# Kernel optimization log

Hardware: AMD Instinct MI355X
Metric: run time of the kernel (lower is better)

The kernel has to match this reference:

```python
import jax, jax.numpy as jnp
import numpy as np
from jax import lax

B, CIN, CH, HW, K = 256, 256, 256, 16, 3


def setup_inputs() -> dict:
    key = jax.random.key(0)
    ks = jax.random.split(key, 9)
    s = 0.05
    return {
        "x": jax.random.normal(ks[0], (B, CIN, HW, HW), dtype=jnp.float32),
        "h": jax.random.normal(ks[1], (B, CH, HW, HW), dtype=jnp.float32),
        "c": jax.random.normal(ks[2], (B, CH, HW, HW), dtype=jnp.float32),
        # stacked x-branch conv weights for gates [i, f, c, o]; no bias (matches torch code)
        "Wx": jax.random.normal(ks[3], (4 * CH, CIN, K, K), dtype=jnp.float32) * s,
        # stacked h-branch conv weights for gates [i, f, c, o]; with bias
        "Wh": jax.random.normal(ks[4], (4 * CH, CH, K, K), dtype=jnp.float32) * s,
        "bh": jax.random.normal(ks[5], (4 * CH,), dtype=jnp.float32) * s,
        # peephole params (torch inits them to zeros; use small randn to exercise the math)
        "Wci": jax.random.normal(ks[6], (1, CH, HW, HW), dtype=jnp.float32) * s,
        "Wcf": jax.random.normal(ks[7], (1, CH, HW, HW), dtype=jnp.float32) * s,
        "Wco": jax.random.normal(ks[8], (1, CH, HW, HW), dtype=jnp.float32) * s,
    }


def _conv(x, w):
    # same-padding 2D conv, NCHW/OIHW
    return lax.conv_general_dilated(
        x, w, window_strides=(1, 1), padding="SAME",
        dimension_numbers=("NCHW", "OIHW", "NCHW"))


def reference(x, h, c, Wx, Wh, bh, Wci, Wcf, Wco):
    gx = _conv(x, Wx)                                   # [B, 4*CH, H, W]
    gh = _conv(h, Wh) + bh[None, :, None, None]         # [B, 4*CH, H, W]
    xi, xf, xc, xo = jnp.split(gx, 4, axis=1)
    hi, hf, hc, ho = jnp.split(gh, 4, axis=1)
    i_t = jax.nn.sigmoid(xi + hi + Wci * c)
    f_t = jax.nn.sigmoid(xf + hf + Wcf * c)
    c_t = f_t * c + i_t * jnp.tanh(xc + hc)
    o_t = jax.nn.sigmoid(xo + ho + Wco * c_t)
    h_t = o_t * jnp.tanh(c_t)
    return (h_t, c_t)
```

## Files before the change

### kernel.cpp

```cpp
#include <hip/hip_runtime.h>


typedef __bf16 bf16x8 __attribute__((ext_vector_type(8)));
typedef float f32x16 __attribute__((ext_vector_type(16)));

#define PLANE_B  20736u
#define XH_BYTES (4096u * PLANE_B)
#define OUT_HALF 16777216u

__device__ inline void gload_lds16(const void* g, void* l) {
    __builtin_amdgcn_global_load_lds(
        (const __attribute__((address_space(1))) void*)g,
        (__attribute__((address_space(3))) void*)l, 16, 0, 0);
}

__global__ __launch_bounds__(256) void xh_transform(
    const float* __restrict__ x, const float* __restrict__ hh,
    unsigned char* __restrict__ xh)
{
    int blk = blockIdx.x;
    int b = blk >> 4, ibk = blk & 15;
    const float* src = (ibk < 8) ? (x  + ((size_t)(b*256 + ibk*32)) * 256)
                                 : (hh + ((size_t)(b*256 + (ibk-8)*32)) * 256);
    int t = threadIdx.x;
    uint32_t w[16];
#pragma unroll
    for (int i = 0; i < 16; ++i) {
        __bf16 lo = (__bf16)src[(size_t)(2*i  )*256 + t];
        __bf16 hi = (__bf16)src[(size_t)(2*i+1)*256 + t];
        w[i] = (uint32_t)__builtin_bit_cast(unsigned short, lo)
             | ((uint32_t)__builtin_bit_cast(unsigned short, hi) << 16);
    }
    unsigned char* plane = xh + (size_t)blk * PLANE_B;
    int p = ((t >> 4) + 1)*18 + (t & 15) + 1;
    uint32_t key  = (uint32_t)(p & 7) << 4;
    uint32_t base = (uint32_t)p * 64u;
#pragma unroll
    for (int k = 0; k < 4; ++k)
        *(uint4*)(plane + ((base + 16u*k) ^ key)) =
            uint4{w[4*k], w[4*k+1], w[4*k+2], w[4*k+3]};
    if (t < 68) {
        int pb;
        if      (t < 18) pb = t;
        else if (t < 36) pb = 17*18 + (t - 18);
        else if (t < 52) pb = (t - 35)*18;
        else             pb = (t - 51)*18 + 17;
        uint32_t kb = (uint32_t)(pb & 7) << 4;
        uint32_t bb = (uint32_t)pb * 64u;
        uint4 z{0u,0u,0u,0u};
#pragma unroll
        for (int k = 0; k < 4; ++k)
            *(uint4*)(plane + ((bb + 16u*k) ^ kb)) = z;
    }
}

__global__ __launch_bounds__(256) void w_transform(
    const float* __restrict__ Wx, const float* __restrict__ Wh,
    __bf16* __restrict__ Wt)
{
    int idx  = blockIdx.x * 256 + threadIdx.x;
    int lane = idx & 63;
    int chunk = idx >> 6;
    int half  = chunk & 1;
    int icblk = (chunk >> 1) & 15;
    int fg    = (chunk >> 5) & 3;
    int cb    = (chunk >> 7) & 7;
    int pos   = chunk >> 10;
    int row = lane & 31, hl = lane >> 5;
    int gate = row & 3, ch8 = row >> 2;
    int oc  = gate*256 + cb*32 + fg*8 + ch8;
    int ic0 = icblk*32 + half*16 + hl*8;
    bf16x8 v;
#pragma unroll
    for (int j = 0; j < 8; ++j) {
        int ic = ic0 + j;
        float w = (ic < 256) ? Wx[((size_t)oc*256 + ic      )*9 + pos]
                             : Wh[((size_t)oc*256 + (ic-256))*9 + pos];
        v[j] = (__bf16)w;
    }
    *(bf16x8*)(Wt + (size_t)chunk*512 + (size_t)lane*8) = v;
}

__global__ __launch_bounds__(256, 3) void convlstm_main(
    const unsigned char* __restrict__ xh, const __bf16* __restrict__ Wt,
    const float* __restrict__ bh,  const float* __restrict__ cin,
    const float* __restrict__ Wci, const float* __restrict__ Wcf,
    const float* __restrict__ Wco, float* __restrict__ out)
{
    int bid = blockIdx.x;
    int cb  = bid & 7;
    int nh  = (bid >> 3) & 1;
    int b   = bid >> 4;
    int tid = threadIdx.x;
    int lane = tid & 63, wv = tid >> 6;
    int l31 = lane & 31, hl = lane >> 5;

    __shared__ __align__(16) unsigned char lds[2][24576];

    f32x16 acc[2][2];
#pragma unroll
    for (int f = 0; f < 2; ++f) {
        int fg = nh*2 + f;
        f32x16 v;
#pragma unroll
        for (int r = 0; r < 16; ++r) {
            int gate = r & 3, q = r >> 2;
            v[r] = bh[gate*256 + cb*32 + fg*8 + 2*q + hl];
        }
        acc[0][f] = v; acc[1][f] = v;
    }

    const unsigned char* planes = xh + (size_t)b * (16u * PLANE_B);

#pragma unroll
    for (int k = 0; k < 6; ++k)
        gload_lds16(planes + (size_t)(wv*6 + k)*1024u + (size_t)lane*16u,
                    &lds[0][(wv*6 + k)*1024 + lane*16]);

    int m0 = wv*64 + l31,       m1 = wv*64 + 32 + l31;
    int pbase0 = (m0 >> 4)*18 + (m0 & 15);
    int pbase1 = (m1 >> 4)*18 + (m1 & 15);
    const uint32_t kbase = (uint32_t)(hl*16);

    const __bf16* wlane = Wt + (size_t)lane * 8;
    auto achunk = [&](int ibk, int ph, int f) -> size_t {
        int pos = ph >> 1, half = ph & 1, fg = nh*2 + f;
        return ((size_t)((pos*8 + cb)*4 + fg))*32 + (size_t)(ibk*2 + half);
    };
    auto bread = [&](const unsigned char* rb, int pbase, int ph) -> bf16x8 {
        int pos = ph >> 1, half = ph & 1;
        int p = pbase + (pos/3)*18 + (pos%3);
        uint32_t byte = ((uint32_t)p*64u + kbase + (uint32_t)(half*32))
                        ^ (((uint32_t)(p & 7)) << 4);
        return *(const bf16x8*)(rb + byte);
    };

    __syncthreads();

    bf16x8 A[2][2];
    A[0][0] = *(const bf16x8*)(wlane + achunk(0, 0, 0)*512);
    A[0][1] = *(const bf16x8*)(wlane + achunk(0, 0, 1)*512);

    for (int ibk = 0; ibk < 16; ++ibk) {
        const int cur = ibk & 1;
        if (ibk < 15) {
            const unsigned char* np = planes + (size_t)(ibk+1) * PLANE_B;
#pragma unroll
            for (int k = 0; k < 6; ++k)
                gload_lds16(np + (size_t)(wv*6 + k)*1024u + (size_t)lane*16u,
                            &lds[cur ^ 1][(wv*6 + k)*1024 + lane*16]);
        }
        const unsigned char* rb = lds[cur];

        bf16x8 Bb[2][2];
        Bb[0][0] = bread(rb, pbase0, 0);
        Bb[0][1] = bread(rb, pbase1, 0);

#pragma unroll
        for (int ph = 0; ph < 18; ++ph) {
            {
                int nib = (ph < 17) ? ibk : ((ibk < 15) ? ibk + 1 : ibk);
                int nph = (ph < 17) ? ph + 1 : 0;
                A[(ph+1)&1][0] = *(const bf16x8*)(wlane + achunk(nib, nph, 0)*512);
                A[(ph+1)&1][1] = *(const bf16x8*)(wlane + achunk(nib, nph, 1)*512);
            }
            if (ph < 17) {
                Bb[(ph+1)&1][0] = bread(rb, pbase0, ph+1);
                Bb[(ph+1)&1][1] = bread(rb, pbase1, ph+1);
            }
            __builtin_amdgcn_s_setprio(1);
            acc[0][0] = __builtin_amdgcn_mfma_f32_32x32x16_bf16(A[ph&1][0], Bb[ph&1][0], acc[0][0], 0, 0, 0);
            acc[0][1] = __builtin_amdgcn_mfma_f32_32x32x16_bf16(A[ph&1][1], Bb[ph&1][0], acc[0][1], 0, 0, 0);
            acc[1][0] = __builtin_amdgcn_mfma_f32_32x32x16_bf16(A[ph&1][0], Bb[ph&1][1], acc[1][0], 0, 0, 0);
            acc[1][1] = __builtin_amdgcn_mfma_f32_32x32x16_bf16(A[ph&1][1], Bb[ph&1][1], acc[1][1], 0, 0, 0);
            __builtin_amdgcn_s_setprio(0);
        }
        __syncthreads();
    }

    float* outh = out;
    float* outc = out + (size_t)OUT_HALF;
    const size_t bOff = (size_t)b * (256*256);
#pragma unroll
    for (int mf = 0; mf < 2; ++mf) {
        int m = wv*64 + mf*32 + l31;
#pragma unroll
        for (int f = 0; f < 2; ++f) {
            int fg = nh*2 + f;
#pragma unroll
            for (int q = 0; q < 4; ++q) {
                int ch = cb*32 + fg*8 + 2*q + hl;
                size_t pidx = (size_t)ch*256 + (size_t)m;
                size_t idx  = bOff + pidx;
                float cv = cin[idx];
                float pi = acc[mf][f][4*q+0];
                float pf = acc[mf][f][4*q+1];
                float pc = acc[mf][f][4*q+2];
                float po = acc[mf][f][4*q+3];
                float it = 1.f/(1.f + __expf(-(pi + Wci[pidx]*cv)));
                float ft = 1.f/(1.f + __expf(-(pf + Wcf[pidx]*cv)));
                float tc = 1.f - 2.f/(1.f + __expf(2.f*pc));
                float ct = ft*cv + it*tc;
                float ot = 1.f/(1.f + __expf(-(po + Wco[pidx]*ct)));
                float th = 1.f - 2.f/(1.f + __expf(2.f*ct));
                outh[idx] = ot*th;
                outc[idx] = ct;
            }
        }
    }
}

extern "C" void kernel_launch(void* const* d_in, const int* in_sizes, int n_in,
                              void* d_out, int out_size, void* d_ws, size_t ws_size,
                              hipStream_t stream)
{
    const float* x   = (const float*)d_in[0];
    const float* h   = (const float*)d_in[1];
    const float* c   = (const float*)d_in[2];
    const float* Wx  = (const float*)d_in[3];
    const float* Wh  = (const float*)d_in[4];
    const float* bh  = (const float*)d_in[5];
    const float* Wci = (const float*)d_in[6];
    const float* Wcf = (const float*)d_in[7];
    const float* Wco = (const float*)d_in[8];
    float* out = (float*)d_out;

    unsigned char* xh = (unsigned char*)d_ws;
    __bf16* Wt = (__bf16*)(xh + (size_t)XH_BYTES + 4096);

    hipLaunchKernelGGL(xh_transform, dim3(4096), dim3(256), 0, stream, x, h, xh);
    hipLaunchKernelGGL(w_transform,  dim3(2304), dim3(256), 0, stream, Wx, Wh, Wt);
    hipLaunchKernelGGL(convlstm_main, dim3(4096), dim3(256), 0, stream,
                       xh, Wt, bh, c, Wci, Wcf, Wco, out);
}
```

Baseline: 640.2 us.

## Deepen weight prefetch, delay plane DMA issue, and use a lighter loop barrier

Weight fragments are now prefetched two MFMA steps ahead through a 3-slot register ring instead of one step ahead. The global-to-LDS load of the next input plane is issued at the second inner step rather than at the top of the channel-block loop. The full __syncthreads at the end of each block becomes an explicit s_waitcnt vmcnt(4) lgkmcnt(0) plus s_barrier, so the still-pending weight prefetches need not drain. Launch bounds drop the minimum blocks per CU from 3 to 2, giving the compiler more registers for the deeper pipeline at the cost of occupancy. The hand-counted vmcnt relies on exactly four weight loads being issued after the DMA loads, which is fragile if the compiler reorders them.

```diff
diff --git a/kernel.cpp b/kernel.cpp
--- a/kernel.cpp
+++ b/kernel.cpp
@@ -81,7 +81,7 @@
     *(bf16x8*)(Wt + (size_t)chunk*512 + (size_t)lane*8) = v;
 }
 
-__global__ __launch_bounds__(256, 3) void convlstm_main(
+__global__ __launch_bounds__(256, 2) void convlstm_main(
     const unsigned char* __restrict__ xh, const __bf16* __restrict__ Wt,
     const float* __restrict__ bh,  const float* __restrict__ cin,
     const float* __restrict__ Wci, const float* __restrict__ Wcf,
@@ -135,47 +135,56 @@
         return *(const bf16x8*)(rb + byte);
     };
 
+    bf16x8 A[3][2];
+#pragma unroll
+    for (int f = 0; f < 2; ++f) {
+        A[0][f] = *(const bf16x8*)(wlane + achunk(0, 0, f)*512);
+        A[1][f] = *(const bf16x8*)(wlane + achunk(0, 1, f)*512);
+    }
+
     __syncthreads();
 
-    bf16x8 A[2][2];
-    A[0][0] = *(const bf16x8*)(wlane + achunk(0, 0, 0)*512);
-    A[0][1] = *(const bf16x8*)(wlane + achunk(0, 0, 1)*512);
-
     for (int ibk = 0; ibk < 16; ++ibk) {
-        const int cur = ibk & 1;
-        if (ibk < 15) {
-            const unsigned char* np = planes + (size_t)(ibk+1) * PLANE_B;
-#pragma unroll
-            for (int k = 0; k < 6; ++k)
-                gload_lds16(np + (size_t)(wv*6 + k)*1024u + (size_t)lane*16u,
-                            &lds[cur ^ 1][(wv*6 + k)*1024 + lane*16]);
-        }
-        const unsigned char* rb = lds[cur];
+        const unsigned char* rb = lds[ibk & 1];
 
         bf16x8 Bb[2][2];
         Bb[0][0] = bread(rb, pbase0, 0);
         Bb[0][1] = bread(rb, pbase1, 0);
 
 #pragma unroll
-        for (int ph = 0; ph < 18; ++ph) {
+        for (int p = 0; p < 18; ++p) {
             {
-                int nib = (ph < 17) ? ibk : ((ibk < 15) ? ibk + 1 : ibk);
-                int nph = (ph < 17) ? ph + 1 : 0;
-                A[(ph+1)&1][0] = *(const bf16x8*)(wlane + achunk(nib, nph, 0)*512);
-                A[(ph+1)&1][1] = *(const bf16x8*)(wlane + achunk(nib, nph, 1)*512);
-            }
-            if (ph < 17) {
-                Bb[(ph+1)&1][0] = bread(rb, pbase0, ph+1);
-                Bb[(ph+1)&1][1] = bread(rb, pbase1, ph+1);
+                int tp  = p + 2;
+                int nib = (tp < 18) ? ibk : ((ibk < 15) ? ibk + 1 : 15);
+                int nph = (tp < 18) ? tp : tp - 18;
+#pragma unroll
+                for (int f = 0; f < 2; ++f)
+                    A[(p+2)%3][f] =
+                        *(const bf16x8*)(wlane + achunk(nib, nph, f)*512);
+            }
+            if (p == 1 && ibk < 15) {
+                const unsigned char* np = planes + (size_t)(ibk+1) * PLANE_B;
+#pragma unroll
+                for (int k = 0; k < 6; ++k)
+                    gload_lds16(np + (size_t)(wv*6 + k)*1024u
+                                   + (size_t)lane*16u,
+                                &lds[(ibk & 1) ^ 1][(wv*6 + k)*1024 + lane*16]);
+            }
+            if (p < 17) {
+                Bb[(p+1)&1][0] = bread(rb, pbase0, p+1);
+                Bb[(p+1)&1][1] = bread(rb, pbase1, p+1);
             }
             __builtin_amdgcn_s_setprio(1);
-            acc[0][0] = __builtin_amdgcn_mfma_f32_32x32x16_bf16(A[ph&1][0], Bb[ph&1][0], acc[0][0], 0, 0, 0);
-            acc[0][1] = __builtin_amdgcn_mfma_f32_32x32x16_bf16(A[ph&1][1], Bb[ph&1][0], acc[0][1], 0, 0, 0);
-            acc[1][0] = __builtin_amdgcn_mfma_f32_32x32x16_bf16(A[ph&1][0], Bb[ph&1][1], acc[1][0], 0, 0, 0);
-            acc[1][1] = __builtin_amdgcn_mfma_f32_32x32x16_bf16(A[ph&1][1], Bb[ph&1][1], acc[1][1], 0, 0, 0);
+            acc[0][0] = __builtin_amdgcn_mfma_f32_32x32x16_bf16(A[p%3][0], Bb[p&1][0], acc[0][0], 0, 0, 0);
+            acc[0][1] = __builtin_amdgcn_mfma_f32_32x32x16_bf16(A[p%3][1], Bb[p&1][0], acc[0][1], 0, 0, 0);
+            acc[1][0] = __builtin_amdgcn_mfma_f32_32x32x16_bf16(A[p%3][0], Bb[p&1][1], acc[1][0], 0, 0, 0);
+            acc[1][1] = __builtin_amdgcn_mfma_f32_32x32x16_bf16(A[p%3][1], Bb[p&1][1], acc[1][1], 0, 0, 0);
             __builtin_amdgcn_s_setprio(0);
         }
-        __syncthreads();
+
+        asm volatile("s_waitcnt vmcnt(4) lgkmcnt(0)" ::: "memory");
+        __builtin_amdgcn_s_barrier();
+        __builtin_amdgcn_sched_barrier(0);
     }
 
     float* outh = out;
```

Result: faster. 626.4 us (-2.2%).
